# Kernel optimization log

Hardware: AMD Instinct MI355X
Metric: run time of the kernel (lower is better)

## Reference

```python
import jax, jax.numpy as jnp
import numpy as np

B, N, D = 8, 2048, 256
K = 8
NP = 1024  # num_pooled = ceil(N * 0.5)
EPS = 1e-8
TEMP = 1.0


def setup_inputs() -> dict:
    key = jax.random.key(0)
    k1, k2, k3, k4 = jax.random.split(key, 4)
    tokens = jax.random.normal(k1, (B, N, D), dtype=jnp.float32)
    timestamps = jax.random.uniform(k2, (B, N), dtype=jnp.float32)
    W1 = jax.random.normal(k3, (2 * D, 128), dtype=jnp.float32) * 0.02
    b1 = jnp.zeros((128,), dtype=jnp.float32)
    W2 = jax.random.normal(k4, (128, NP), dtype=jnp.float32) * 0.02
    b2 = jnp.zeros((NP,), dtype=jnp.float32)
    return {"tokens": tokens, "timestamps": timestamps, "W1": W1, "b1": b1, "W2": W2, "b2": b2}


def _build_adjacency(tokens):
    # mutual-kNN graph on cosine similarity -> [B, N, N] float 0/1
    tn = tokens / (jnp.linalg.norm(tokens, axis=-1, keepdims=True) + EPS)
    sim = jnp.einsum("bnd,bmd->bnm", tn, tn)
    sim = jnp.where(jnp.eye(N, dtype=bool)[None], -jnp.inf, sim)  # no self (add_self=False)
    _, idx = jax.lax.top_k(sim, K)  # [B, N, K]
    bi = jnp.arange(B)[:, None, None]
    ri = jnp.arange(N)[None, :, None]
    adj = jnp.zeros((B, N, N), dtype=bool).at[bi, ri, idx].set(True)
    adj = adj & jnp.swapaxes(adj, 1, 2)  # mutual
    return adj.astype(jnp.float32)


def reference(tokens, timestamps, W1, b1, W2, b2):
    adjacency = _build_adjacency(tokens)

    # degree-normalized aggregation (use_gnn=True)
    degree = jnp.clip(adjacency.sum(axis=-1, keepdims=True), 1.0, None)
    agg = jnp.matmul(adjacency / degree, tokens)  # [B, N, D]
    features = jnp.concatenate([tokens, agg], axis=-1)  # [B, N, 2D]

    # assignment MLP (Linear -> exact GELU -> Linear), softmax over clusters
    h = jax.nn.gelu(features @ W1 + b1, approximate=False)
    logits = h @ W2 + b2  # [B, N, NP]
    assign = jax.nn.softmax(logits / TEMP, axis=-1)

    # soft-assignment pooling
    pooled_tokens = jnp.einsum("bnp,bnd->bpd", assign, tokens)  # [B, NP, D]
    pooled_t = jnp.einsum("bnp,bn->bp", assign, timestamps)  # [B, NP]

    # reorder pooled tokens by pooled timestamp
    sort_idx = jnp.argsort(pooled_t, axis=-1)
    pooled_tokens = jnp.take_along_axis(pooled_tokens, sort_idx[..., None], axis=1)
    pooled_t = jnp.take_along_axis(pooled_t, sort_idx, axis=1)

    # auxiliary losses
    assign_st = jnp.einsum("bnp,bmp->bnm", assign, assign)
    link_loss = jnp.mean((assign_st - adjacency) ** 2)
    entropy = jnp.mean(-jnp.sum(assign * jnp.log(assign + EPS), axis=-1))

    return pooled_tokens, pooled_t, link_loss, entropy
```

## Files before the change

kernel.cpp:

```cpp
#include <hip/hip_runtime.h>
#include <math.h>

#define B_ 8
#define N_ 2048
#define D_ 256
#define K_ 8
#define NP_ 1024
#define H_ 128
#define EPS_ 1e-8f
#define NEG_INF_ (-1e30f)

typedef unsigned int uint;
typedef unsigned short ushort;
typedef __attribute__((ext_vector_type(4))) float f32x4;
typedef __attribute__((ext_vector_type(8))) short short8;

__device__ __forceinline__ float gelu_exact(float x) {
    return 0.5f * x * (1.0f + erff(x * 0.70710678118654752440f));
}

__device__ __forceinline__ float dot4(float4 a, float4 b) {
    return a.x * b.x + a.y * b.y + a.z * b.z + a.w * b.w;
}

__device__ __forceinline__ ushort f2bf(float f) {
    uint u = __float_as_uint(f);
    u = (u + 0x7FFFu + ((u >> 16) & 1u)) >> 16;
    return (ushort)u;
}

__device__ __forceinline__ void gll16(const void* g, void* l) {
    __builtin_amdgcn_global_load_lds(
        (const __attribute__((address_space(1))) unsigned int*)g,
        (__attribute__((address_space(3))) unsigned int*)l, 16, 0, 0);
}

__device__ __forceinline__ float bsum256(float* red, int t, float v) {
    red[t] = v;
    __syncthreads();
#pragma unroll
    for (int s = 128; s > 0; s >>= 1) {
        if (t < s) red[t] += red[t + s];
        __syncthreads();
    }
    float r = red[0];
    __syncthreads();
    return r;
}

__device__ __forceinline__ float bmax256(float* red, int t, float v) {
    red[t] = v;
    __syncthreads();
#pragma unroll
    for (int s = 128; s > 0; s >>= 1) {
        if (t < s) red[t] = fmaxf(red[t], red[t + s]);
        __syncthreads();
    }
    float r = red[0];
    __syncthreads();
    return r;
}

__device__ __forceinline__ uint mono16(uint v) {
    return (v & 0x8000u) ? ((~v) & 0xFFFFu) : (v | 0x8000u);
}

__global__ __launch_bounds__(256) void k_norm(const float* __restrict__ tokens,
                                              float* __restrict__ tn,
                                              ushort* __restrict__ tnbf) {
    int row = blockIdx.x;
    int t = threadIdx.x;
    __shared__ float red[256];
    float x = tokens[(size_t)row * D_ + t];
    float ss = bsum256(red, t, x * x);
    float nrm = sqrtf(ss) + EPS_;
    float y = x / nrm;
    tn[(size_t)row * D_ + t] = y;
    tnbf[(size_t)row * D_ + t] = f2bf(y);
}

#define INSK_(L) { bool in_ = key > L; uint tm_ = L; L = in_ ? key : L; key = in_ ? tm_ : key; }
#define INS16_ INSK_(l0) INSK_(l1) INSK_(l2) INSK_(l3) INSK_(l4) INSK_(l5) INSK_(l6) INSK_(l7) \
               INSK_(l8) INSK_(l9) INSK_(l10) INSK_(l11) INSK_(l12) INSK_(l13) INSK_(l14) INSK_(l15)
#define INSM_ INSK_(m0) INSK_(m1) INSK_(m2) INSK_(m3) INSK_(m4) INSK_(m5) INSK_(m6) INSK_(m7) \
              INSK_(m8) INSK_(m9) INSK_(m10) INSK_(m11) INSK_(m12) INSK_(m13) INSK_(m14) INSK_(m15)

__global__ __launch_bounds__(256) void k_simtop(const ushort* __restrict__ tnbf,
                                                int* __restrict__ cands) {
    __shared__ __align__(16) char lds[53504];
    char* Bs = lds + 16384;
    ushort* sc = (ushort*)(lds + 49152);
    uint* mg = (uint*)(lds + 16384);

    int bid = blockIdx.x;
    int b = bid & 7;
    int panel = bid >> 3;
    int i0 = panel * 32;
    int t = threadIdx.x;
    int lane = t & 63;
    int wv = t >> 6;
    int rh = wv & 1, ch = wv >> 1;
    const char* tbb = (const char*)(tnbf + (size_t)b * N_ * D_);

#pragma unroll
    for (int c = 0; c < 4; ++c) {
        int e = (wv * 4 + c) * 64 + lane;
        int row = e >> 5, g = e & 31;
        gll16(tbb + (size_t)(i0 + row) * 512 + ((g ^ ((row & 7) << 2)) << 4),
              lds + (wv * 4 + c) * 1024);
    }
#pragma unroll
    for (int c = 0; c < 8; ++c) {
        int e = (wv * 8 + c) * 64 + lane;
        int row = e >> 5, g = e & 31;
        gll16(tbb + (size_t)row * 512 + ((g ^ ((row & 7) << 2)) << 4),
              Bs + (wv * 8 + c) * 1024);
    }
    asm volatile("s_waitcnt vmcnt(0)" ::: "memory");
    __syncthreads();

    int selrow = t >> 3;
    int selcs = t & 7;
    int gi = i0 + selrow;
    uint l0=0,l1=0,l2=0,l3=0,l4=0,l5=0,l6=0,l7=0,l8=0,l9=0,l10=0,l11=0,l12=0,l13=0,l14=0,l15=0;

    int arow = rh * 16 + (lane & 15);
    int brow0 = ch * 32 + (lane & 15);
    int brow1 = brow0 + 16;
    int aoff = arow * 512;
    int ax = (arow & 7) << 2;
    int bx0 = (brow0 & 7) << 2;
    int bx1 = (brow1 & 7) << 2;
    int scw = (rh * 16 + (lane >> 4) * 4) * 66 + ch * 32 + (lane & 15);

    for (int jt = 0; jt < 32; ++jt) {
        f32x4 acc0 = (f32x4){0.f,0.f,0.f,0.f};
        f32x4 acc1 = (f32x4){0.f,0.f,0.f,0.f};
#pragma unroll
        for (int ks = 0; ks < 8; ++ks) {
            int u = ks * 4 + (lane >> 4);
            short8 af = *(const short8*)(lds + aoff + ((u ^ ax) << 4));
            short8 bf0 = *(const short8*)(Bs + brow0 * 512 + ((u ^ bx0) << 4));
            short8 bf1 = *(const short8*)(Bs + brow1 * 512 + ((u ^ bx1) << 4));
            acc0 = __builtin_amdgcn_mfma_f32_16x16x32_bf16(af, bf0, acc0, 0, 0, 0);
            acc1 = __builtin_amdgcn_mfma_f32_16x16x32_bf16(af, bf1, acc1, 0, 0, 0);
        }
#pragma unroll
        for (int v = 0; v < 4; ++v) sc[scw + v * 66] = f2bf(acc0[v]);
#pragma unroll
        for (int v = 0; v < 4; ++v) sc[scw + v * 66 + 16] = f2bf(acc1[v]);
        __syncthreads();

        if (jt < 31) {
#pragma unroll
            for (int c = 0; c < 8; ++c) {
                int e = (wv * 8 + c) * 64 + lane;
                int row = e >> 5, g = e & 31;
                gll16(tbb + (size_t)((jt + 1) * 64 + row) * 512 + ((g ^ ((row & 7) << 2)) << 4),
                      Bs + (wv * 8 + c) * 1024);
            }
        }
        int j0 = jt * 64;
        int sbase = selrow * 66;
#pragma unroll
        for (int jj = 0; jj < 8; ++jj) {
            int col = selcs + jj * 8;
            int j = j0 + col;
            uint sv = sc[sbase + col];
            if (j != gi) {
                uint key = (mono16(sv) << 16) | (65535u - (uint)j);
                if (key > l15) { INS16_ }
            }
        }
        asm volatile("s_waitcnt vmcnt(0)" ::: "memory");
        __syncthreads();
    }

    uint* ml = mg + (size_t)t * 17;
    ml[0]=l0; ml[1]=l1; ml[2]=l2; ml[3]=l3; ml[4]=l4; ml[5]=l5; ml[6]=l6; ml[7]=l7;
    ml[8]=l8; ml[9]=l9; ml[10]=l10; ml[11]=l11; ml[12]=l12; ml[13]=l13; ml[14]=l14; ml[15]=l15;
    __syncthreads();
    if (selcs == 0) {
        uint m0=0,m1=0,m2=0,m3=0,m4=0,m5=0,m6=0,m7=0,m8=0,m9=0,m10=0,m11=0,m12=0,m13=0,m14=0,m15=0;
        const uint* base = mg + (size_t)(selrow * 8) * 17;
#pragma unroll
        for (int s2 = 0; s2 < 8; ++s2) {
            const uint* lp = base + s2 * 17;
            for (int q = 0; q < 16; ++q) {
                uint key = lp[q];
                if (key <= m15) break;
                INSM_
            }
        }
        int* crow = cands + ((size_t)b * N_ + gi) * 16;
        crow[0]=(int)(65535u-(m0&0xFFFFu));   crow[1]=(int)(65535u-(m1&0xFFFFu));
        crow[2]=(int)(65535u-(m2&0xFFFFu));   crow[3]=(int)(65535u-(m3&0xFFFFu));
        crow[4]=(int)(65535u-(m4&0xFFFFu));   crow[5]=(int)(65535u-(m5&0xFFFFu));
        crow[6]=(int)(65535u-(m6&0xFFFFu));   crow[7]=(int)(65535u-(m7&0xFFFFu));
        crow[8]=(int)(65535u-(m8&0xFFFFu));   crow[9]=(int)(65535u-(m9&0xFFFFu));
        crow[10]=(int)(65535u-(m10&0xFFFFu)); crow[11]=(int)(65535u-(m11&0xFFFFu));
        crow[12]=(int)(65535u-(m12&0xFFFFu)); crow[13]=(int)(65535u-(m13&0xFFFFu));
        crow[14]=(int)(65535u-(m14&0xFFFFu)); crow[15]=(int)(65535u-(m15&0xFFFFu));
    }
}

__global__ __launch_bounds__(64) void k_rescore(const float* __restrict__ tn,
                                                const int* __restrict__ cands,
                                                int* __restrict__ topk) {
    int row = blockIdx.x;
    int b = row >> 11;
    int lane = threadIdx.x;
    int j = cands[(size_t)row * 16 + (lane & 15)];
    float s = 0.f;
    if (lane < 16) {
        const float* ti = tn + (size_t)row * D_;
        const float* tj = tn + ((size_t)(b << 11) + j) * D_;
        for (int d = 0; d < D_; d += 4) {
            float4 u = *(const float4*)(tj + d);
            float4 w = *(const float4*)(ti + d);
            s += dot4(u, w);
        }
    }
    float dv[16];
    int jv[16];
#pragma unroll
    for (int c = 0; c < 16; ++c) {
        dv[c] = __shfl(s, c);
        jv[c] = __shfl(j, c);
    }
    uint used = 0;
    for (int r = 0; r < 8; ++r) {
        float bv = -1e38f;
        int bj = 1 << 30, bc = -1;
#pragma unroll
        for (int c = 0; c < 16; ++c) {
            bool av = !(used & (1u << c));
            bool better = av && (dv[c] > bv || (dv[c] == bv && jv[c] < bj));
            bv = better ? dv[c] : bv;
            bj = better ? jv[c] : bj;
            bc = better ? c : bc;
        }
        used |= 1u << bc;
        if (lane == 0) topk[(size_t)row * K_ + r] = bj;
    }
}

__global__ __launch_bounds__(64) void k_adj_agg(const float* __restrict__ tokens,
                                                const int* __restrict__ topk,
                                                int* __restrict__ nbr,
                                                int* __restrict__ deg,
                                                float* __restrict__ agg) {
    int row = blockIdx.x;
    int b = row >> 11;
    int i = row & (N_ - 1);
    int t = threadIdx.x;
    __shared__ int s_cand[K_];
    __shared__ int s_nbr[K_];
    __shared__ int s_deg;
    if (t < K_) {
        int j = topk[(size_t)row * K_ + t];
        const int* tj = topk + ((size_t)(b * N_ + j)) * K_;
        bool mut = false;
#pragma unroll
        for (int k = 0; k < K_; ++k) mut = mut || (tj[k] == i);
        s_cand[t] = mut ? j : -1;
    }
    __syncthreads();
    if (t == 0) {
        int d = 0;
#pragma unroll
        for (int k = 0; k < K_; ++k)
            if (s_cand[k] >= 0) s_nbr[d++] = s_cand[k];
        s_deg = d;
    }
    __syncthreads();
    int dgi = s_deg;
    const float* tb = tokens + (size_t)b * N_ * D_;
    float a0 = 0, a1 = 0, a2 = 0, a3 = 0;
    for (int k = 0; k < dgi; ++k) {
        float4 v = *(const float4*)(tb + (size_t)s_nbr[k] * D_ + t * 4);
        a0 += v.x; a1 += v.y; a2 += v.z; a3 += v.w;
    }
    float inv = 1.0f / (float)(dgi > 0 ? dgi : 1);
    *(float4*)(agg + (size_t)row * D_ + t * 4) = make_float4(a0 * inv, a1 * inv, a2 * inv, a3 * inv);
    if (t < K_) nbr[(size_t)row * K_ + t] = (t < dgi) ? s_nbr[t] : -1;
    if (t == 0) deg[row] = dgi;
}

__global__ __launch_bounds__(256) void k_tokT(const float* __restrict__ tokens,
                                              ushort* __restrict__ tokT) {
    int b = blockIdx.z;
    int n0 = blockIdx.x * 32, d0 = blockIdx.y * 32;
    __shared__ float tile[32][33];
    int t = threadIdx.x;
#pragma unroll
    for (int q = 0; q < 4; ++q) {
        int e = q * 256 + t;
        int r = e >> 5, c = e & 31;
        tile[r][c] = tokens[((size_t)b * N_ + n0 + r) * D_ + d0 + c];
    }
    __syncthreads();
#pragma unroll
    for (int q = 0; q < 4; ++q) {
        int e = q * 256 + t;
        int r = e >> 5, c = e & 31;
        tokT[((size_t)b * D_ + d0 + r) * N_ + n0 + c] = f2bf(tile[c][r]);
    }
}

__global__ __launch_bounds__(256) void k_asT(const float* __restrict__ assign,
                                             ushort* __restrict__ assignT) {
    int b = blockIdx.z;
    int n0 = blockIdx.x * 32, p0 = blockIdx.y * 32;
    __shared__ float tile[32][33];
    int t = threadIdx.x;
#pragma unroll
    for (int q = 0; q < 4; ++q) {
        int e = q * 256 + t;
        int r = e >> 5, c = e & 31;
        tile[r][c] = assign[((size_t)b * N_ + n0 + r) * NP_ + p0 + c];
    }
    __syncthreads();
#pragma unroll
    for (int q = 0; q < 4; ++q) {
        int e = q * 256 + t;
        int r = e >> 5, c = e & 31;
        assignT[((size_t)b * NP_ + p0 + r) * N_ + n0 + c] = f2bf(tile[c][r]);
    }
}

__global__ __launch_bounds__(256) void k_mlp1(const float* __restrict__ tokens,
                                              const float* __restrict__ agg,
                                              const float* __restrict__ W1,
                                              const float* __restrict__ b1,
                                              float* __restrict__ h) {
    int row0 = blockIdx.x * 16;
    int t = threadIdx.x;
    int col = t & 127;
    int half = t >> 7;
    __shared__ float feat[16][2 * D_];
    for (int e = t; e < 16 * 2 * D_; e += 256) {
        int r = e >> 9, c = e & 511;
        feat[r][c] = (c < D_) ? tokens[(size_t)(row0 + r) * D_ + c]
                              : agg[(size_t)(row0 + r) * D_ + (c - D_)];
    }
    __syncthreads();
    const float* fr = &feat[half * 8][0];
    float bias = b1[col];
    float a0 = bias, a1 = bias, a2 = bias, a3 = bias, a4 = bias, a5 = bias, a6 = bias, a7 = bias;
    for (int i = 0; i < 2 * D_; i += 4) {
        float w0 = W1[(size_t)(i + 0) * H_ + col];
        float w1 = W1[(size_t)(i + 1) * H_ + col];
        float w2 = W1[(size_t)(i + 2) * H_ + col];
        float w3 = W1[(size_t)(i + 3) * H_ + col];
        float4 f0 = *(const float4*)(fr + 0 * 512 + i);
        float4 f1 = *(const float4*)(fr + 1 * 512 + i);
        float4 f2 = *(const float4*)(fr + 2 * 512 + i);
        float4 f3 = *(const float4*)(fr + 3 * 512 + i);
        float4 f4 = *(const float4*)(fr + 4 * 512 + i);
        float4 f5 = *(const float4*)(fr + 5 * 512 + i);
        float4 f6 = *(const float4*)(fr + 6 * 512 + i);
        float4 f7 = *(const float4*)(fr + 7 * 512 + i);
        a0 += f0.x * w0; a0 += f0.y * w1; a0 += f0.z * w2; a0 += f0.w * w3;
        a1 += f1.x * w0; a1 += f1.y * w1; a1 += f1.z * w2; a1 += f1.w * w3;
        a2 += f2.x * w0; a2 += f2.y * w1; a2 += f2.z * w2; a2 += f2.w * w3;
        a3 += f3.x * w0; a3 += f3.y * w1; a3 += f3.z * w2; a3 += f3.w * w3;
        a4 += f4.x * w0; a4 += f4.y * w1; a4 += f4.z * w2; a4 += f4.w * w3;
        a5 += f5.x * w0; a5 += f5.y * w1; a5 += f5.z * w2; a5 += f5.w * w3;
        a6 += f6.x * w0; a6 += f6.y * w1; a6 += f6.z * w2; a6 += f6.w * w3;
        a7 += f7.x * w0; a7 += f7.y * w1; a7 += f7.z * w2; a7 += f7.w * w3;
    }
    int rb = row0 + half * 8;
    h[(size_t)(rb + 0) * H_ + col] = gelu_exact(a0);
    h[(size_t)(rb + 1) * H_ + col] = gelu_exact(a1);
    h[(size_t)(rb + 2) * H_ + col] = gelu_exact(a2);
    h[(size_t)(rb + 3) * H_ + col] = gelu_exact(a3);
    h[(size_t)(rb + 4) * H_ + col] = gelu_exact(a4);
    h[(size_t)(rb + 5) * H_ + col] = gelu_exact(a5);
    h[(size_t)(rb + 6) * H_ + col] = gelu_exact(a6);
    h[(size_t)(rb + 7) * H_ + col] = gelu_exact(a7);
}

__global__ __launch_bounds__(256) void k_logits(const float* __restrict__ hmat,
                                                const float* __restrict__ W2,
                                                const float* __restrict__ b2,
                                                float* __restrict__ logits) {
    int bid = blockIdx.x;
    int row0 = (bid >> 2) * 16;
    int col = (bid & 3) * 256 + threadIdx.x;
    int t = threadIdx.x;
    __shared__ float hs[16][H_];
    for (int e = t; e < 16 * H_; e += 256) hs[e >> 7][e & 127] = hmat[(size_t)row0 * H_ + e];
    __syncthreads();
    float acc[16];
    float bb = b2[col];
#pragma unroll
    for (int r = 0; r < 16; ++r) acc[r] = bb;
    for (int i = 0; i < H_; ++i) {
        float w = W2[(size_t)i * NP_ + col];
#pragma unroll
        for (int r = 0; r < 16; ++r) acc[r] += hs[r][i] * w;
    }
#pragma unroll
    for (int r = 0; r < 16; ++r) logits[(size_t)(row0 + r) * NP_ + col] = acc[r];
}

__global__ __launch_bounds__(256) void k_softmax(float* __restrict__ assign,
                                                 float* __restrict__ ent_partial) {
    int row0 = blockIdx.x * 8;
    int t = threadIdx.x;
    __shared__ float red[256];
    float entv = 0.f;
#pragma unroll
    for (int r = 0; r < 8; ++r) {
        float* arow = assign + (size_t)(row0 + r) * NP_;
        float a0 = arow[t], a1 = arow[256 + t], a2 = arow[512 + t], a3 = arow[768 + t];
        float m = bmax256(red, t, fmaxf(fmaxf(a0, a1), fmaxf(a2, a3)));
        float e0 = expf(a0 - m), e1 = expf(a1 - m), e2 = expf(a2 - m), e3 = expf(a3 - m);
        float tot = bsum256(red, t, e0 + e1 + e2 + e3);
        float inv = 1.0f / tot;
        float p0 = e0 * inv, p1 = e1 * inv, p2 = e2 * inv, p3 = e3 * inv;
        arow[t] = p0; arow[256 + t] = p1; arow[512 + t] = p2; arow[768 + t] = p3;
        entv -= p0 * logf(p0 + EPS_) + p1 * logf(p1 + EPS_) + p2 * logf(p2 + EPS_) + p3 * logf(p3 + EPS_);
    }
    float bs = bsum256(red, t, entv);
    if (t == 0) ent_partial[blockIdx.x] = bs;
}

__device__ __forceinline__ void stage8k(const ushort* __restrict__ A,
                                        const ushort* __restrict__ B,
                                        int kb, char* lA, char* lB, int wv, int lane) {
#pragma unroll
    for (int c = 0; c < 2; ++c) {
        int e = (wv * 2 + c) * 64 + lane;
        int row = e >> 3, g = e & 7;
        size_t go = (size_t)row * N_ + kb + ((g ^ (row & 7)) << 3);
        gll16(A + go, lA + (wv * 2 + c) * 1024);
        gll16(B + go, lB + (wv * 2 + c) * 1024);
    }
}

__device__ __forceinline__ void gemm64g(const ushort* __restrict__ A,
                                        const ushort* __restrict__ B,
                                        f32x4 acc[2][2], char* lds) {
    int t = threadIdx.x;
    int lane = t & 63;
    int wv = t >> 6;
    int wm = wv >> 1, wn = wv & 1;
    stage8k(A, B, 0, lds, lds + 8192, wv, lane);
    for (int kb = 0; kb < N_; kb += 64) {
        int cur = (kb >> 6) & 1;
        char* lA = lds + cur * 16384;
        char* lB = lA + 8192;
        asm volatile("s_waitcnt vmcnt(0)" ::: "memory");
        __syncthreads();
        if (kb + 64 < N_) {
            char* nA = lds + (cur ^ 1) * 16384;
            stage8k(A, B, kb + 64, nA, nA + 8192, wv, lane);
        }
#pragma unroll
        for (int ks = 0; ks < 2; ++ks) {
            short8 afr[2], bfr[2];
#pragma unroll
            for (int f = 0; f < 2; ++f) {
                int rowA = wm * 32 + f * 16 + (lane & 15);
                int u = ks * 4 + (lane >> 4);
                afr[f] = *(const short8*)(lA + rowA * 128 + ((u ^ (rowA & 7)) << 4));
                int rowB = wn * 32 + f * 16 + (lane & 15);
                bfr[f] = *(const short8*)(lB + rowB * 128 + ((u ^ (rowB & 7)) << 4));
            }
#pragma unroll
            for (int fm = 0; fm < 2; ++fm)
#pragma unroll
                for (int fn = 0; fn < 2; ++fn)
                    acc[fm][fn] = __builtin_amdgcn_mfma_f32_16x16x32_bf16(
                        afr[fm], bfr[fn], acc[fm][fn], 0, 0, 0);
        }
    }
}

__global__ __launch_bounds__(256) void k_pool64(const ushort* __restrict__ assignT,
                                                const ushort* __restrict__ tokT,
                                                float* __restrict__ pooled) {
    __shared__ __align__(16) char lds[32768];
    int bid = blockIdx.x;
    int b = bid & 7;
    int tile = bid >> 3;
    int p0 = (tile >> 2) * 64, d0 = (tile & 3) * 64;
    const ushort* A = assignT + ((size_t)b * NP_ + p0) * N_;
    const ushort* Bp = tokT + ((size_t)b * D_ + d0) * N_;
    f32x4 acc[2][2];
#pragma unroll
    for (int x = 0; x < 2; ++x)
#pragma unroll
        for (int y = 0; y < 2; ++y) acc[x][y] = (f32x4){0.f, 0.f, 0.f, 0.f};
    gemm64g(A, Bp, acc, lds);
    int lane = threadIdx.x & 63;
    int wid = threadIdx.x >> 6;
    int wm = wid >> 1, wn = wid & 1;
#pragma unroll
    for (int fm = 0; fm < 2; ++fm)
#pragma unroll
        for (int fn = 0; fn < 2; ++fn) {
            int p = p0 + wm * 32 + fm * 16 + (lane >> 4) * 4;
            int d = d0 + wn * 32 + fn * 16 + (lane & 15);
#pragma unroll
            for (int v = 0; v < 4; ++v)
                pooled[((size_t)b * NP_ + p + v) * D_ + d] = acc[fm][fn][v];
        }
}

__global__ __launch_bounds__(256) void k_gram64(const ushort* __restrict__ assignT,
                                                float* __restrict__ gram_partial) {
    __shared__ __align__(16) char lds[32768];
    __shared__ float red[256];
    int bid = blockIdx.x;
    int b = bid & 7;
    int idx = bid >> 3;
    int ti = 0, rem = idx;
    while (rem >= 16 - ti) { rem -= 16 - ti; ++ti; }
    int tj = ti + rem;
    const ushort* A = assignT + ((size_t)b * NP_ + ti * 64) * N_;
    const ushort* Bp = assignT + ((size_t)b * NP_ + tj * 64) * N_;
    f32x4 acc[2][2];
#pragma unroll
    for (int x = 0; x < 2; ++x)
#pragma unroll
        for (int y = 0; y < 2; ++y) acc[x][y] = (f32x4){0.f, 0.f, 0.f, 0.f};
    gemm64g(A, Bp, acc, lds);
    float lsum = 0.f;
#pragma unroll
    for (int x = 0; x < 2; ++x)
#pragma unroll
        for (int y = 0; y < 2; ++y)
#pragma unroll
            for (int v = 0; v < 4; ++v) lsum += acc[x][y][v] * acc[x][y][v];
    float bs = bsum256(red, threadIdx.x, lsum);
    if (threadIdx.x == 0) gram_partial[(size_t)b * 136 + idx] = (ti == tj ? 1.0f : 2.0f) * bs;
}

__global__ __launch_bounds__(256) void k_poolt_part(const float* __restrict__ assign,
                                                    const float* __restrict__ ts,
                                                    float* __restrict__ part) {
    int bid = blockIdx.x;
    int b = bid & 7, ck = bid >> 3;
    int t = threadIdx.x;
    const float* A = assign + ((size_t)b * N_ + (size_t)ck * 64) * NP_;
    const float* T = ts + (size_t)b * N_ + (size_t)ck * 64;
    float4 acc = make_float4(0.f, 0.f, 0.f, 0.f);
    for (int n = 0; n < 64; ++n) {
        float4 v = *(const float4*)(A + (size_t)n * NP_ + t * 4);
        float tv = T[n];
        acc.x += v.x * tv; acc.y += v.y * tv; acc.z += v.z * tv; acc.w += v.w * tv;
    }
    *(float4*)(part + ((size_t)(b * 32 + ck)) * NP_ + t * 4) = acc;
}

__global__ __launch_bounds__(256) void k_poolt_red(const float* __restrict__ part,
                                                   float* __restrict__ pooled_t_u) {
    int b = blockIdx.x;
    int t = threadIdx.x;
    float4 acc = make_float4(0.f, 0.f, 0.f, 0.f);
    for (int ck = 0; ck < 32; ++ck) {
        float4 v = *(const float4*)(part + ((size_t)(b * 32 + ck)) * NP_ + t * 4);
        acc.x += v.x; acc.y += v.y; acc.z += v.z; acc.w += v.w;
    }
    *(float4*)(pooled_t_u + (size_t)b * NP_ + t * 4) = acc;
}

__global__ __launch_bounds__(64) void k_edge(const float* __restrict__ assign,
                                             const int* __restrict__ nbr,
                                             const int* __restrict__ deg,
                                             float* __restrict__ edge_partial) {
    int row = blockIdx.x;
    int t = threadIdx.x;
    int dgi = deg[row];
    int b = row >> 11;
    float acc = 0.f;
    if (dgi > 0) {
        const float* ai = assign + (size_t)row * NP_;
        float areg[16];
#pragma unroll
        for (int q = 0; q < 16; ++q) areg[q] = ai[q * 64 + t];
        for (int k = 0; k < dgi; ++k) {
            int j = nbr[(size_t)row * K_ + k];
            const float* aj = assign + ((size_t)(b * N_ + j)) * NP_;
#pragma unroll
            for (int q = 0; q < 16; ++q) acc += areg[q] * aj[q * 64 + t];
        }
    }
#pragma unroll
    for (int s = 32; s > 0; s >>= 1) acc += __shfl_down(acc, s);
    if (t == 0) edge_partial[row] = acc;
}

__global__ __launch_bounds__(256) void k_sort(const float* __restrict__ pooled_t_u,
                                              float* __restrict__ out_pt,
                                              int* __restrict__ sortidx) {
    int b = blockIdx.x;
    int t = threadIdx.x;
    __shared__ float val[NP_];
    __shared__ int sidx[NP_];
    for (int e = t; e < NP_; e += 256) { val[e] = pooled_t_u[(size_t)b * NP_ + e]; sidx[e] = e; }
    __syncthreads();
    for (int k = 2; k <= NP_; k <<= 1) {
        for (int j = k >> 1; j > 0; j >>= 1) {
            for (int e = t; e < NP_; e += 256) {
                int l = e ^ j;
                if (l > e) {
                    bool up = ((e & k) == 0);
                    float v1 = val[e], v2 = val[l];
                    int i1 = sidx[e], i2 = sidx[l];
                    bool sw = up ? ((v1 > v2) || (v1 == v2 && i1 > i2))
                                 : ((v1 < v2) || (v1 == v2 && i1 < i2));
                    if (sw) { val[e] = v2; val[l] = v1; sidx[e] = i2; sidx[l] = i1; }
                }
            }
            __syncthreads();
        }
    }
    for (int e = t; e < NP_; e += 256) {
        out_pt[(size_t)b * NP_ + e] = val[e];
        sortidx[(size_t)b * NP_ + e] = sidx[e];
    }
}

__global__ __launch_bounds__(64) void k_gather(const float* __restrict__ pooledU,
                                               const int* __restrict__ sortidx,
                                               float* __restrict__ out) {
    int bp = blockIdx.x;
    int b = bp >> 10;
    int src = sortidx[bp];
    const float4* s = (const float4*)(pooledU + ((size_t)(b << 10) + src) * D_);
    float4* d = (float4*)(out + (size_t)bp * D_);
    d[threadIdx.x] = s[threadIdx.x];
}

__global__ __launch_bounds__(256) void k_fin(const float* __restrict__ gram_partial,
                                             const float* __restrict__ edge_partial,
                                             const float* __restrict__ ent_partial,
                                             const int* __restrict__ deg,
                                             float* __restrict__ out2) {
    int t = threadIdx.x;
    __shared__ float red[256];
    float t1 = 0.f, t2 = 0.f, t3 = 0.f, ent = 0.f;
    for (int i = t; i < 136 * B_; i += 256) t1 += gram_partial[i];
    for (int i = t; i < B_ * N_; i += 256) t2 += edge_partial[i];
    for (int i = t; i < (B_ * N_) / 8; i += 256) ent += ent_partial[i];
    for (int i = t; i < B_ * N_; i += 256) t3 += (float)deg[i];
    t1 = bsum256(red, t, t1);
    t2 = bsum256(red, t, t2);
    t3 = bsum256(red, t, t3);
    ent = bsum256(red, t, ent);
    if (t == 0) {
        out2[0] = (t1 - 2.f * t2 + t3) / (float)((size_t)B_ * N_ * N_);
        out2[1] = ent / (float)(B_ * N_);
    }
}

extern "C" void kernel_launch(void* const* d_in, const int* in_sizes, int n_in,
                              void* d_out, int out_size, void* d_ws, size_t ws_size,
                              hipStream_t stream) {
    const float* tokens = (const float*)d_in[0];
    const float* tstamp = (const float*)d_in[1];
    const float* W1 = (const float*)d_in[2];
    const float* b1 = (const float*)d_in[3];
    const float* W2 = (const float*)d_in[4];
    const float* b2 = (const float*)d_in[5];
    float* out = (float*)d_out;

    char* wsp = (char*)d_ws;
    size_t off = 0;
    auto alloc = [&](size_t bytes) -> void* {
        void* p = wsp + off;
        off += (bytes + 255) & ~(size_t)255;
        return p;
    };
    float* tn = (float*)alloc(sizeof(float) * (size_t)B_ * N_ * D_);
    float* agg = tn;
    float* assign = (float*)alloc(sizeof(float) * (size_t)B_ * N_ * NP_);
    ushort* tnbf = (ushort*)alloc(sizeof(ushort) * (size_t)B_ * N_ * D_);
    ushort* tokT = tnbf;
    float* hbuf = (float*)alloc(sizeof(float) * (size_t)B_ * N_ * H_);
    ushort* assignT = (ushort*)alloc(sizeof(ushort) * (size_t)B_ * NP_ * N_);
    float* pooledU = (float*)alloc(sizeof(float) * (size_t)B_ * NP_ * D_);
    float* pooltU = (float*)alloc(sizeof(float) * (size_t)B_ * NP_);
    float* poolt_part = (float*)alloc(sizeof(float) * (size_t)B_ * 32 * NP_);
    int* candbuf = (int*)alloc(sizeof(int) * (size_t)B_ * N_ * 16);
    int* topkbuf = (int*)alloc(sizeof(int) * (size_t)B_ * N_ * K_);
    int* nbrbuf = (int*)alloc(sizeof(int) * (size_t)B_ * N_ * K_);
    int* degbuf = (int*)alloc(sizeof(int) * (size_t)B_ * N_);
    int* sortidx = (int*)alloc(sizeof(int) * (size_t)B_ * NP_);
    float* gram_p = (float*)alloc(sizeof(float) * 136 * B_);
    float* edge_p = (float*)alloc(sizeof(float) * (size_t)B_ * N_);
    float* ent_p = (float*)alloc(sizeof(float) * (size_t)(B_ * N_) / 8);

    k_norm<<<B_ * N_, 256, 0, stream>>>(tokens, tn, tnbf);
    k_simtop<<<512, 256, 0, stream>>>(tnbf, candbuf);
    k_rescore<<<B_ * N_, 64, 0, stream>>>(tn, candbuf, topkbuf);
    k_adj_agg<<<B_ * N_, 64, 0, stream>>>(tokens, topkbuf, nbrbuf, degbuf, agg);
    k_tokT<<<dim3(N_ / 32, D_ / 32, B_), 256, 0, stream>>>(tokens, tokT);
    k_mlp1<<<(B_ * N_) / 16, 256, 0, stream>>>(tokens, agg, W1, b1, hbuf);
    k_logits<<<(B_ * N_) / 16 * 4, 256, 0, stream>>>(hbuf, W2, b2, assign);
    k_softmax<<<(B_ * N_) / 8, 256, 0, stream>>>(assign, ent_p);
    k_asT<<<dim3(N_ / 32, NP_ / 32, B_), 256, 0, stream>>>(assign, assignT);
    k_pool64<<<512, 256, 0, stream>>>(assignT, tokT, pooledU);
    k_poolt_part<<<256, 256, 0, stream>>>(assign, tstamp, poolt_part);
    k_poolt_red<<<B_, 256, 0, stream>>>(poolt_part, pooltU);
    k_gram64<<<1088, 256, 0, stream>>>(assignT, gram_p);
    k_edge<<<B_ * N_, 64, 0, stream>>>(assign, nbrbuf, degbuf, edge_p);
    k_sort<<<B_, 256, 0, stream>>>(pooltU, out + (size_t)B_ * NP_ * D_, sortidx);
    k_gather<<<B_ * NP_, 64, 0, stream>>>(pooledU, sortidx, out);
    k_fin<<<1, 256, 0, stream>>>(gram_p, edge_p, ent_p, degbuf,
                                 out + (size_t)B_ * NP_ * D_ + (size_t)B_ * NP_);
}
```

Baseline: 624.6 us.

## Fuse logits GEMM with softmax and halve simtop row panel

The separate logits kernel and softmax kernel are merged, so each block computes all 1024 logits for 16 rows in registers and applies softmax and entropy directly. This removes one full write and read of the B×N×NP logits tensor through global memory. Separately, the similarity/top-k kernel now uses 16-row panels with one MFMA tile per wave and twice as many blocks, with a new XOR swizzle and padded score stride. The trade-off is more register pressure (64 accumulators) in the fused kernel and more redundant B-tile loads in simtop.

```diff
diff --git a/kernel.cpp b/kernel.cpp
--- a/kernel.cpp
+++ b/kernel.cpp
@@ -79,6 +79,7 @@
     tnbf[(size_t)row * D_ + t] = f2bf(y);
 }
 
+#define SCW_ 72
 #define INSK_(L) { bool in_ = key > L; uint tm_ = L; L = in_ ? key : L; key = in_ ? tm_ : key; }
 #define INS16_ INSK_(l0) INSK_(l1) INSK_(l2) INSK_(l3) INSK_(l4) INSK_(l5) INSK_(l6) INSK_(l7) \
                INSK_(l8) INSK_(l9) INSK_(l10) INSK_(l11) INSK_(l12) INSK_(l13) INSK_(l14) INSK_(l15)
@@ -87,68 +88,57 @@
 
 __global__ __launch_bounds__(256) void k_simtop(const ushort* __restrict__ tnbf,
                                                 int* __restrict__ cands) {
-    __shared__ __align__(16) char lds[53504];
-    char* Bs = lds + 16384;
-    ushort* sc = (ushort*)(lds + 49152);
-    uint* mg = (uint*)(lds + 16384);
+    __shared__ __align__(16) char lds[43264];
+    char* Bs = lds + 8192;
+    ushort* sc = (ushort*)(lds + 40960);
+    uint* mg = (uint*)(lds + 8192);
 
     int bid = blockIdx.x;
     int b = bid & 7;
     int panel = bid >> 3;
-    int i0 = panel * 32;
+    int i0 = panel * 16;
     int t = threadIdx.x;
     int lane = t & 63;
     int wv = t >> 6;
-    int rh = wv & 1, ch = wv >> 1;
     const char* tbb = (const char*)(tnbf + (size_t)b * N_ * D_);
 
 #pragma unroll
-    for (int c = 0; c < 4; ++c) {
-        int e = (wv * 4 + c) * 64 + lane;
+    for (int c = 0; c < 2; ++c) {
+        int e = (wv * 2 + c) * 64 + lane;
         int row = e >> 5, g = e & 31;
-        gll16(tbb + (size_t)(i0 + row) * 512 + ((g ^ ((row & 7) << 2)) << 4),
-              lds + (wv * 4 + c) * 1024);
+        gll16(tbb + (size_t)(i0 + row) * 512 + ((g ^ (row & 15)) << 4),
+              lds + (wv * 2 + c) * 1024);
     }
 #pragma unroll
     for (int c = 0; c < 8; ++c) {
         int e = (wv * 8 + c) * 64 + lane;
         int row = e >> 5, g = e & 31;
-        gll16(tbb + (size_t)row * 512 + ((g ^ ((row & 7) << 2)) << 4),
+        gll16(tbb + (size_t)row * 512 + ((g ^ (row & 15)) << 4),
               Bs + (wv * 8 + c) * 1024);
     }
     asm volatile("s_waitcnt vmcnt(0)" ::: "memory");
     __syncthreads();
 
-    int selrow = t >> 3;
-    int selcs = t & 7;
+    int selrow = t >> 4;
+    int selcs = t & 15;
     int gi = i0 + selrow;
     uint l0=0,l1=0,l2=0,l3=0,l4=0,l5=0,l6=0,l7=0,l8=0,l9=0,l10=0,l11=0,l12=0,l13=0,l14=0,l15=0;
 
-    int arow = rh * 16 + (lane & 15);
-    int brow0 = ch * 32 + (lane & 15);
-    int brow1 = brow0 + 16;
-    int aoff = arow * 512;
-    int ax = (arow & 7) << 2;
-    int bx0 = (brow0 & 7) << 2;
-    int bx1 = (brow1 & 7) << 2;
-    int scw = (rh * 16 + (lane >> 4) * 4) * 66 + ch * 32 + (lane & 15);
+    int arow = lane & 15;
+    int brow = wv * 16 + (lane & 15);
+    int scw = ((lane >> 4) * 4) * SCW_ + wv * 16 + (lane & 15);
 
     for (int jt = 0; jt < 32; ++jt) {
-        f32x4 acc0 = (f32x4){0.f,0.f,0.f,0.f};
-        f32x4 acc1 = (f32x4){0.f,0.f,0.f,0.f};
+        f32x4 acc = (f32x4){0.f, 0.f, 0.f, 0.f};
 #pragma unroll
         for (int ks = 0; ks < 8; ++ks) {
             int u = ks * 4 + (lane >> 4);
-            short8 af = *(const short8*)(lds + aoff + ((u ^ ax) << 4));
-            short8 bf0 = *(const short8*)(Bs + brow0 * 512 + ((u ^ bx0) << 4));
-            short8 bf1 = *(const short8*)(Bs + brow1 * 512 + ((u ^ bx1) << 4));
-            acc0 = __builtin_amdgcn_mfma_f32_16x16x32_bf16(af, bf0, acc0, 0, 0, 0);
-            acc1 = __builtin_amdgcn_mfma_f32_16x16x32_bf16(af, bf1, acc1, 0, 0, 0);
-        }
-#pragma unroll
-        for (int v = 0; v < 4; ++v) sc[scw + v * 66] = f2bf(acc0[v]);
-#pragma unroll
-        for (int v = 0; v < 4; ++v) sc[scw + v * 66 + 16] = f2bf(acc1[v]);
+            short8 af = *(const short8*)(lds + arow * 512 + ((u ^ arow) << 4));
+            short8 bf = *(const short8*)(Bs + brow * 512 + ((u ^ (lane & 15)) << 4));
+            acc = __builtin_amdgcn_mfma_f32_16x16x32_bf16(af, bf, acc, 0, 0, 0);
+        }
+#pragma unroll
+        for (int v = 0; v < 4; ++v) sc[scw + v * SCW_] = f2bf(acc[v]);
         __syncthreads();
 
         if (jt < 31) {
@@ -156,15 +146,15 @@
             for (int c = 0; c < 8; ++c) {
                 int e = (wv * 8 + c) * 64 + lane;
                 int row = e >> 5, g = e & 31;
-                gll16(tbb + (size_t)((jt + 1) * 64 + row) * 512 + ((g ^ ((row & 7) << 2)) << 4),
+                gll16(tbb + (size_t)((jt + 1) * 64 + row) * 512 + ((g ^ (row & 15)) << 4),
                       Bs + (wv * 8 + c) * 1024);
             }
         }
         int j0 = jt * 64;
-        int sbase = selrow * 66;
-#pragma unroll
-        for (int jj = 0; jj < 8; ++jj) {
-            int col = selcs + jj * 8;
+        int sbase = selrow * SCW_;
+#pragma unroll
+        for (int jj = 0; jj < 4; ++jj) {
+            int col = selcs + jj * 16;
             int j = j0 + col;
             uint sv = sc[sbase + col];
             if (j != gi) {
@@ -182,9 +172,9 @@
     __syncthreads();
     if (selcs == 0) {
         uint m0=0,m1=0,m2=0,m3=0,m4=0,m5=0,m6=0,m7=0,m8=0,m9=0,m10=0,m11=0,m12=0,m13=0,m14=0,m15=0;
-        const uint* base = mg + (size_t)(selrow * 8) * 17;
-#pragma unroll
-        for (int s2 = 0; s2 < 8; ++s2) {
+        const uint* base = mg + (size_t)(selrow * 16) * 17;
+#pragma unroll
+        for (int s2 = 0; s2 < 16; ++s2) {
             const uint* lp = base + s2 * 17;
             for (int q = 0; q < 16; ++q) {
                 uint key = lp[q];
@@ -381,45 +371,54 @@
     h[(size_t)(rb + 7) * H_ + col] = gelu_exact(a7);
 }
 
-__global__ __launch_bounds__(256) void k_logits(const float* __restrict__ hmat,
-                                                const float* __restrict__ W2,
-                                                const float* __restrict__ b2,
-                                                float* __restrict__ logits) {
-    int bid = blockIdx.x;
-    int row0 = (bid >> 2) * 16;
-    int col = (bid & 3) * 256 + threadIdx.x;
-    int t = threadIdx.x;
-    __shared__ float hs[16][H_];
-    for (int e = t; e < 16 * H_; e += 256) hs[e >> 7][e & 127] = hmat[(size_t)row0 * H_ + e];
-    __syncthreads();
-    float acc[16];
-    float bb = b2[col];
-#pragma unroll
-    for (int r = 0; r < 16; ++r) acc[r] = bb;
+__global__ __launch_bounds__(256) void k_mlp2f(const float* __restrict__ hmat,
+                                               const float* __restrict__ W2,
+                                               const float* __restrict__ b2,
+                                               float* __restrict__ assign,
+                                               float* __restrict__ ent_partial) {
+    int row0 = blockIdx.x * 16;
+    int t = threadIdx.x;
+    __shared__ float hsT[128 * 17];
+    __shared__ float red[256];
+    for (int e = t; e < 16 * H_; e += 256) {
+        int r = e >> 7, i = e & 127;
+        hsT[i * 17 + r] = hmat[(size_t)row0 * H_ + e];
+    }
+    __syncthreads();
+    float acc[16][4];
+#pragma unroll
+    for (int s = 0; s < 4; ++s) {
+        float bb = b2[s * 256 + t];
+#pragma unroll
+        for (int r = 0; r < 16; ++r) acc[r][s] = bb;
+    }
+#pragma unroll 2
     for (int i = 0; i < H_; ++i) {
-        float w = W2[(size_t)i * NP_ + col];
-#pragma unroll
-        for (int r = 0; r < 16; ++r) acc[r] += hs[r][i] * w;
-    }
-#pragma unroll
-    for (int r = 0; r < 16; ++r) logits[(size_t)(row0 + r) * NP_ + col] = acc[r];
-}
-
-__global__ __launch_bounds__(256) void k_softmax(float* __restrict__ assign,
-                                                 float* __restrict__ ent_partial) {
-    int row0 = blockIdx.x * 8;
-    int t = threadIdx.x;
-    __shared__ float red[256];
+        float w0 = W2[(size_t)i * NP_ + t];
+        float w1 = W2[(size_t)i * NP_ + 256 + t];
+        float w2 = W2[(size_t)i * NP_ + 512 + t];
+        float w3 = W2[(size_t)i * NP_ + 768 + t];
+        float hv[16];
+        *(float4*)&hv[0] = *(const float4*)&hsT[i * 17 + 0];
+        *(float4*)&hv[4] = *(const float4*)&hsT[i * 17 + 4];
+        *(float4*)&hv[8] = *(const float4*)&hsT[i * 17 + 8];
+        *(float4*)&hv[12] = *(const float4*)&hsT[i * 17 + 12];
+#pragma unroll
+        for (int r = 0; r < 16; ++r) {
+            acc[r][0] += hv[r] * w0; acc[r][1] += hv[r] * w1;
+            acc[r][2] += hv[r] * w2; acc[r][3] += hv[r] * w3;
+        }
+    }
     float entv = 0.f;
 #pragma unroll
-    for (int r = 0; r < 8; ++r) {
-        float* arow = assign + (size_t)(row0 + r) * NP_;
-        float a0 = arow[t], a1 = arow[256 + t], a2 = arow[512 + t], a3 = arow[768 + t];
+    for (int r = 0; r < 16; ++r) {
+        float a0 = acc[r][0], a1 = acc[r][1], a2 = acc[r][2], a3 = acc[r][3];
         float m = bmax256(red, t, fmaxf(fmaxf(a0, a1), fmaxf(a2, a3)));
         float e0 = expf(a0 - m), e1 = expf(a1 - m), e2 = expf(a2 - m), e3 = expf(a3 - m);
         float tot = bsum256(red, t, e0 + e1 + e2 + e3);
         float inv = 1.0f / tot;
         float p0 = e0 * inv, p1 = e1 * inv, p2 = e2 * inv, p3 = e3 * inv;
+        float* arow = assign + (size_t)(row0 + r) * NP_;
         arow[t] = p0; arow[256 + t] = p1; arow[512 + t] = p2; arow[768 + t] = p3;
         entv -= p0 * logf(p0 + EPS_) + p1 * logf(p1 + EPS_) + p2 * logf(p2 + EPS_) + p3 * logf(p3 + EPS_);
     }
@@ -646,7 +645,7 @@
     float t1 = 0.f, t2 = 0.f, t3 = 0.f, ent = 0.f;
     for (int i = t; i < 136 * B_; i += 256) t1 += gram_partial[i];
     for (int i = t; i < B_ * N_; i += 256) t2 += edge_partial[i];
-    for (int i = t; i < (B_ * N_) / 8; i += 256) ent += ent_partial[i];
+    for (int i = t; i < (B_ * N_) / 16; i += 256) ent += ent_partial[i];
     for (int i = t; i < B_ * N_; i += 256) t3 += (float)deg[i];
     t1 = bsum256(red, t, t1);
     t2 = bsum256(red, t, t2);
@@ -693,16 +692,15 @@
     int* sortidx = (int*)alloc(sizeof(int) * (size_t)B_ * NP_);
     float* gram_p = (float*)alloc(sizeof(float) * 136 * B_);
     float* edge_p = (float*)alloc(sizeof(float) * (size_t)B_ * N_);
-    float* ent_p = (float*)alloc(sizeof(float) * (size_t)(B_ * N_) / 8);
+    float* ent_p = (float*)alloc(sizeof(float) * (size_t)(B_ * N_) / 16);
 
     k_norm<<<B_ * N_, 256, 0, stream>>>(tokens, tn, tnbf);
-    k_simtop<<<512, 256, 0, stream>>>(tnbf, candbuf);
+    k_simtop<<<1024, 256, 0, stream>>>(tnbf, candbuf);
     k_rescore<<<B_ * N_, 64, 0, stream>>>(tn, candbuf, topkbuf);
     k_adj_agg<<<B_ * N_, 64, 0, stream>>>(tokens, topkbuf, nbrbuf, degbuf, agg);
     k_tokT<<<dim3(N_ / 32, D_ / 32, B_), 256, 0, stream>>>(tokens, tokT);
     k_mlp1<<<(B_ * N_) / 16, 256, 0, stream>>>(tokens, agg, W1, b1, hbuf);
-    k_logits<<<(B_ * N_) / 16 * 4, 256, 0, stream>>>(hbuf, W2, b2, assign);
-    k_softmax<<<(B_ * N_) / 8, 256, 0, stream>>>(assign, ent_p);
+    k_mlp2f<<<(B_ * N_) / 16, 256, 0, stream>>>(hbuf, W2, b2, assign, ent_p);
     k_asT<<<dim3(N_ / 32, NP_ / 32, B_), 256, 0, stream>>>(assign, assignT);
     k_pool64<<<512, 256, 0, stream>>>(assignT, tokT, pooledU);
     k_poolt_part<<<256, 256, 0, stream>>>(assign, tstamp, poolt_part);
```

Result: slower. 673.2 us (+7.8%).
